# Performance work log

Measured on AMD Instinct MI355X. Metric: run time of the kernel, lower is better.

Reference implementation:

```python
import jax, jax.numpy as jnp
import numpy as np

BANDWIDTH = 1.0
DRIFT_COEF = 1.0
NEG_DRIFT_COEF = 0.5
EPS = 1e-8

B, TA, DA = 4096, 16, 8


def setup_inputs() -> dict:
    key = jax.random.key(0)
    k1, k2, k3 = jax.random.split(key, 3)
    x = jax.random.normal(k1, (B, TA, DA), dtype=jnp.float32)
    y_pos = jax.random.normal(k2, (B, TA, DA), dtype=jnp.float32)
    y_neg = jax.random.normal(k3, (B, TA, DA), dtype=jnp.float32)
    return {"x": x, "y_pos": y_pos, "y_neg": y_neg}


def _drift_field(x_flat, y_flat, sign):
    """Nadaraya-Watson weighted average of pairwise diffs, fused via norms+matmul.

    Equivalent to: sign * sum_j wn_ij * (x_i - y_j)
    where wn = row-normalized RBF kernel with masked diagonal.
    """
    b = x_flat.shape[0]
    x_sq = jnp.sum(x_flat * x_flat, axis=1)
    y_sq = jnp.sum(y_flat * y_flat, axis=1)
    d2 = x_sq[:, None] + y_sq[None, :] - 2.0 * (x_flat @ y_flat.T)
    d2 = jnp.maximum(d2, 0.0)
    w = jnp.exp(-d2 / (2.0 * BANDWIDTH ** 2))
    # mask self-interaction (mask_self=True)
    w = w * (1.0 - jnp.eye(b, dtype=w.dtype))
    s = jnp.sum(w, axis=1, keepdims=True)               # (B, 1)
    denom = jnp.maximum(s, EPS)
    wn = w / denom                                       # (B, B)
    # sum_j wn_ij (x_i - y_j) = x_i * rowsum(wn)_i - wn @ y
    diff_avg = x_flat * (s / denom) - wn @ y_flat        # (B, D)
    return sign * diff_avg


def reference(x, y_pos, y_neg):
    b = x.shape[0]
    x_flat = x.reshape(b, -1)
    yp_flat = y_pos.reshape(b, -1)
    yn_flat = y_neg.reshape(b, -1)
    # V_pos = wn_pos @ (-(x_i - y_j)); V_neg = wn_neg @ (x_i - y_j)
    v = DRIFT_COEF * _drift_field(x_flat, yp_flat, -1.0)
    v = v + NEG_DRIFT_COEF * _drift_field(x_flat, yn_flat, 1.0)
    return v.reshape(x.shape)
```

## Files before the change

### kernel.cpp

```cpp
#include <hip/hip_runtime.h>
#include <math.h>


#define EPSV 1e-8f
#define CUTOFF_F 162.0f
#define LCAP 1024

typedef unsigned int uint;
typedef unsigned short ushort;
typedef __attribute__((ext_vector_type(8))) short bf16x8;
typedef __attribute__((ext_vector_type(4))) float f32x4;

#define ACC_IDX 20480u
#define XA_BYTE 8388608u
#define MAT_BYTES 1048576u
#define WS_NEED 11534336u

static __device__ __forceinline__ ushort bf16_rne(float v) {
    uint u = __float_as_uint(v);
    uint r = (u + 0x7FFFu + ((u >> 16) & 1u)) >> 16;
    return (ushort)r;
}

typedef const __attribute__((address_space(1))) uint guint;
typedef __attribute__((address_space(3))) uint luint;
static __device__ __forceinline__ void lds_load16(const void* g, void* l) {
    __builtin_amdgcn_global_load_lds((guint*)g, (luint*)l, 16, 0, 0);
}

__global__ __launch_bounds__(256) void prep_k(
    const float* __restrict__ x, const float* __restrict__ yp,
    const float* __restrict__ yn, float* __restrict__ ws,
    unsigned char* __restrict__ wsb, int build)
{
    __shared__ ushort hi_s[4][128];
    const int t = threadIdx.x, wv = t >> 6, lane = t & 63;
    const int rid = blockIdx.x * 4 + wv;
    const int seg = rid >> 12;
    const int row = rid & 4095;
    const float* src = (seg == 0) ? x : (seg == 1) ? yp : yn;

    float2 v = ((const float2*)(src + (size_t)row * 128))[lane];
    float ss = v.x * v.x + v.y * v.y;
    #pragma unroll
    for (int off = 32; off > 0; off >>= 1) ss += __shfl_down(ss, off);
    if (lane == 0) ws[8192 + seg * 4096 + row] = ss;

    if (build) {
        hi_s[wv][2 * lane]     = bf16_rne(v.x);
        hi_s[wv][2 * lane + 1] = bf16_rne(v.y);
        __syncthreads();
        const int K = 2 * lane;
        const int g = K >> 6, c = (K >> 3) & 7, off = K & 7;
        const int Klog = (g << 6) + ((c ^ (row & 7)) << 3) + off;
        uint* dst = (uint*)(wsb + XA_BYTE + (size_t)seg * MAT_BYTES) + (size_t)row * 64;
        dst[lane] = (uint)hi_s[wv][Klog] | ((uint)hi_s[wv][Klog + 1] << 16);
    }

    const uint gid = blockIdx.x * 256u + (uint)t;
    for (uint u = gid; u < 1056768u; u += 786432u) {
        const uint idx = (u < 8192u) ? u : (u + 12288u);
        ws[idx] = 0.0f;
    }
}

__global__ __launch_bounds__(256) void phase_a_mfma(
    const float* __restrict__ x, const float* __restrict__ yp,
    const float* __restrict__ yn,
    const unsigned char* __restrict__ wsb, float* __restrict__ wsf)
{
    const ushort* __restrict__ XA = (const ushort*)(wsb + XA_BYTE);
    const ushort* __restrict__ YPB = (const ushort*)(wsb + XA_BYTE + MAT_BYTES);
    const ushort* __restrict__ YNB = (const ushort*)(wsb + XA_BYTE + 2u * MAT_BYTES);

    __shared__ ushort As[128 * 128];
    __shared__ ushort Bs[128 * 128];
    __shared__ uint pbuf[LCAP];
    __shared__ uint pcnt;

    const int t = threadIdx.x;
    const int lane = t & 63, wv = t >> 6;
    const int wr = wv >> 1, wc = wv & 1;
    const int i0 = blockIdx.y * 128, j0 = blockIdx.x * 128;
    const int m = lane & 15, qd = lane >> 4;
    const int r4 = lane >> 4, c16 = lane & 15;

    if (t == 0) pcnt = 0;

    #pragma unroll
    for (int q = 0; q < 8; ++q) {
        const int rr = 32 * wv + 4 * q;
        lds_load16(XA + (size_t)(i0 + rr + r4) * 128 + c16 * 8, &As[rr * 128]);
        lds_load16(YPB + (size_t)(j0 + rr + r4) * 128 + c16 * 8, &Bs[rr * 128]);
    }
    __syncthreads();

    float xq[4][4];
    #pragma unroll
    for (int fi = 0; fi < 4; ++fi)
        #pragma unroll
        for (int rg = 0; rg < 4; ++rg)
            xq[fi][rg] = wsf[8192 + i0 + 64 * wr + 16 * fi + 4 * qd + rg];

    auto run_field = [&](const int f) {
        f32x4 acc[4][4];
        #pragma unroll
        for (int a = 0; a < 4; ++a)
            #pragma unroll
            for (int bb = 0; bb < 4; ++bb) acc[a][bb] = (f32x4)0.0f;

        #pragma unroll
        for (int ks = 0; ks < 4; ++ks) {
            const int lc = 4 * ks + qd;
            const int phys = ((lc >> 3) << 3) | ((lc & 7) ^ (m & 7));
            bf16x8 av[4], bv[4];
            #pragma unroll
            for (int ff = 0; ff < 4; ++ff) {
                const int ra = 64 * wr + 16 * ff + m;
                av[ff] = *(const bf16x8*)&As[ra * 128 + phys * 8];
                const int rb = 64 * wc + 16 * ff + m;
                bv[ff] = *(const bf16x8*)&Bs[rb * 128 + phys * 8];
            }
            #pragma unroll
            for (int fi = 0; fi < 4; ++fi)
                #pragma unroll
                for (int fj = 0; fj < 4; ++fj)
                    acc[fi][fj] = __builtin_amdgcn_mfma_f32_16x16x32_bf16(
                        av[fi], bv[fj], acc[fi][fj], 0, 0, 0);
        }

        const float* __restrict__ ysq = wsf + 12288 + f * 4096;
        float yq[4];
        #pragma unroll
        for (int fj = 0; fj < 4; ++fj)
            yq[fj] = ysq[j0 + 64 * wc + 16 * fj + m];

        #pragma unroll
        for (int fi = 0; fi < 4; ++fi) {
            #pragma unroll
            for (int fj = 0; fj < 4; ++fj) {
                #pragma unroll
                for (int rg = 0; rg < 4; ++rg) {
                    const int i = i0 + 64 * wr + 16 * fi + 4 * qd + rg;
                    const int j = j0 + 64 * wc + 16 * fj + m;
                    float d2a = xq[fi][rg] + yq[fj] - 2.0f * acc[fi][fj][rg];
                    if (d2a < CUTOFF_F && i != j) {
                        uint li = atomicAdd(&pcnt, 1u);
                        if (li < LCAP)
                            pbuf[li] = (uint)i | ((uint)j << 12) | ((uint)f << 24);
                    }
                }
            }
        }
    };

    run_field(0);
    __syncthreads();
    #pragma unroll
    for (int q = 0; q < 8; ++q) {
        const int rr = 32 * wv + 4 * q;
        lds_load16(YNB + (size_t)(j0 + rr + r4) * 128 + c16 * 8, &Bs[rr * 128]);
    }
    __syncthreads();
    run_field(1);
    __syncthreads();

    uint n = pcnt; if (n > LCAP) n = LCAP;
    for (uint p = wv; p < n; p += 4) {
        const uint pk = pbuf[p];
        const uint i = pk & 0xFFFu, j = (pk >> 12) & 0xFFFu, fb = (pk >> 24) & 1u;
        const float* __restrict__ Yg = fb ? yn : yp;
        float2 xa = ((const float2*)(x + (size_t)i * 128))[lane];
        float2 yb = ((const float2*)(Yg + (size_t)j * 128))[lane];
        float d = xa.x * yb.x + xa.y * yb.y;
        #pragma unroll
        for (int off = 32; off > 0; off >>= 1) d += __shfl_xor(d, off);
        const float d2 = fmaxf(wsf[8192 + i] + wsf[12288 + fb * 4096u + j] - 2.0f * d, 0.0f);
        const float w = __expf(-0.5f * d2);
        if (lane == 0) atomicAdd(&wsf[fb * 4096u + i], w);
        float* __restrict__ accT = wsf + ACC_IDX + fb * 524288u + (size_t)i * 128u;
        atomicAdd(&accT[2 * lane],     w * yb.x);
        atomicAdd(&accT[2 * lane + 1], w * yb.y);
    }
}

__global__ __launch_bounds__(256) void phase_a_f32(
    const float* __restrict__ x, const float* __restrict__ yp,
    const float* __restrict__ yn, float* __restrict__ ws)
{
    const int f = blockIdx.z;
    const float* __restrict__ Y   = f ? yn : yp;
    const float* __restrict__ xsq = ws + 8192;
    const float* __restrict__ ysq = ws + (f ? 16384 : 12288);
    float* __restrict__ S         = ws + (f ? 4096 : 0);
    float* __restrict__ accT      = ws + ACC_IDX + (size_t)f * 524288u;

    __shared__ float xs[32][128 + 4];
    __shared__ float ys[32][128 + 4];

    const int t  = threadIdx.x;
    const int tx = t & 15, ty = t >> 4;
    const int i0 = blockIdx.y * 128, j0 = blockIdx.x * 128;

    float acc[8][8];
    #pragma unroll
    for (int a = 0; a < 8; ++a)
        #pragma unroll
        for (int bb = 0; bb < 8; ++bb) acc[a][bb] = 0.f;

    const int ldr = t >> 1;
    const int ldk = (t & 1) * 16;

    for (int k0 = 0; k0 < 128; k0 += 32) {
        #pragma unroll
        for (int q = 0; q < 4; ++q) {
            float4 vx = *(const float4*)&x[(size_t)(i0 + ldr) * 128 + k0 + ldk + 4 * q];
            float4 vy = *(const float4*)&Y[(size_t)(j0 + ldr) * 128 + k0 + ldk + 4 * q];
            const int kb = ldk + 4 * q;
            xs[kb + 0][ldr] = vx.x; xs[kb + 1][ldr] = vx.y;
            xs[kb + 2][ldr] = vx.z; xs[kb + 3][ldr] = vx.w;
            ys[kb + 0][ldr] = vy.x; ys[kb + 1][ldr] = vy.y;
            ys[kb + 2][ldr] = vy.z; ys[kb + 3][ldr] = vy.w;
        }
        __syncthreads();
        #pragma unroll 4
        for (int kk = 0; kk < 32; ++kk) {
            float4 a0 = *(const float4*)&xs[kk][8 * ty];
            float4 a1 = *(const float4*)&xs[kk][8 * ty + 4];
            float4 b0 = *(const float4*)&ys[kk][8 * tx];
            float4 b1 = *(const float4*)&ys[kk][8 * tx + 4];
            float av[8] = {a0.x, a0.y, a0.z, a0.w, a1.x, a1.y, a1.z, a1.w};
            float bv[8] = {b0.x, b0.y, b0.z, b0.w, b1.x, b1.y, b1.z, b1.w};
            #pragma unroll
            for (int di = 0; di < 8; ++di)
                #pragma unroll
                for (int dj = 0; dj < 8; ++dj)
                    acc[di][dj] = fmaf(av[di], bv[dj], acc[di][dj]);
        }
        __syncthreads();
    }

    float xqv[8], yqv[8], srow[8];
    #pragma unroll
    for (int di = 0; di < 8; ++di) { xqv[di] = xsq[i0 + 8 * ty + di]; srow[di] = 0.f; }
    #pragma unroll
    for (int dj = 0; dj < 8; ++dj) yqv[dj] = ysq[j0 + 8 * tx + dj];

    #pragma unroll
    for (int di = 0; di < 8; ++di) {
        const int i = i0 + 8 * ty + di;
        #pragma unroll
        for (int dj = 0; dj < 8; ++dj) {
            const int j = j0 + 8 * tx + dj;
            float d2 = fmaxf(xqv[di] + yqv[dj] - 2.0f * acc[di][dj], 0.0f);
            if (i != j) {
                float w = __expf(-0.5f * d2);
                srow[di] += w;
                if (d2 < CUTOFF_F) {
                    const float* Yrow = Y + (size_t)j * 128;
                    for (int k = 0; k < 128; ++k)
                        atomicAdd(&accT[(size_t)i * 128 + k], w * Yrow[k]);
                }
            }
        }
    }
    #pragma unroll
    for (int di = 0; di < 8; ++di) {
        float v = srow[di];
        #pragma unroll
        for (int off = 8; off > 0; off >>= 1) v += __shfl_down(v, off, 16);
        if (tx == 0) atomicAdd(&S[i0 + 8 * ty + di], v);
    }
}

__global__ __launch_bounds__(256) void finalize_k(
    const float* __restrict__ x, const float* __restrict__ ws,
    float* __restrict__ out)
{
    const uint gid = blockIdx.x * 256u + threadIdx.x;
    const uint i = gid >> 7;
    const float spv = ws[i], snv = ws[4096 + i];
    const float denp = fmaxf(spv, EPSV), denn = fmaxf(snv, EPSV);
    const float c = 0.5f * snv / denn - spv / denp;
    out[gid] = x[gid] * c
             + ws[ACC_IDX + gid] / denp
             - 0.5f * ws[ACC_IDX + 524288u + gid] / denn;
}

extern "C" void kernel_launch(void* const* d_in, const int* in_sizes, int n_in,
                              void* d_out, int out_size, void* d_ws, size_t ws_size,
                              hipStream_t stream)
{
    const float* x  = (const float*)d_in[0];
    const float* yp = (const float*)d_in[1];
    const float* yn = (const float*)d_in[2];
    float* out = (float*)d_out;
    float* ws  = (float*)d_ws;
    unsigned char* wsb = (unsigned char*)d_ws;

    const bool use_mfma = (ws_size >= WS_NEED);

    prep_k<<<3072, 256, 0, stream>>>(x, yp, yn, ws, wsb, use_mfma ? 1 : 0);
    if (use_mfma) {
        dim3 ga(32, 32, 1);
        phase_a_mfma<<<ga, 256, 0, stream>>>(x, yp, yn, wsb, ws);
    } else {
        dim3 ga(32, 32, 2);
        phase_a_f32<<<ga, 256, 0, stream>>>(x, yp, yn, ws);
    }
    finalize_k<<<2048, 256, 0, stream>>>(x, ws, out);
}
```

Before: 103.0 us.

## Convert fp32 to bf16 inside MFMA tile kernel and split fields across grid z

Removes the prep-stage build of pre-swizzled bf16 copies of x, y_pos and y_neg in workspace. The MFMA distance kernel now reads fp32 rows directly, rounds them to bf16 in registers, and stages two K-halves through smaller LDS tiles. The two fields move to separate blocks via blockIdx.z, and launch bounds are tightened for occupancy. This drops a global write/read round trip and lowers LDS use per block, but x tiles are converted twice and the candidate list cap is halved, which risks overflow if a tile has many close pairs.

Measured after the change: 101.2 us (median of 2 runs). Within noise of the previous version (-1.7%).

```diff
diff --git a/kernel.cpp b/kernel.cpp
--- a/kernel.cpp
+++ b/kernel.cpp
@@ -4,7 +4,7 @@
 
 #define EPSV 1e-8f
 #define CUTOFF_F 162.0f
-#define LCAP 1024
+#define LCAP 512
 
 typedef unsigned int uint;
 typedef unsigned short ushort;
@@ -12,9 +12,7 @@
 typedef __attribute__((ext_vector_type(4))) float f32x4;
 
 #define ACC_IDX 20480u
-#define XA_BYTE 8388608u
-#define MAT_BYTES 1048576u
-#define WS_NEED 11534336u
+#define WS_NEED 4276224u
 
 static __device__ __forceinline__ ushort bf16_rne(float v) {
     uint u = __float_as_uint(v);
@@ -22,18 +20,10 @@
     return (ushort)r;
 }
 
-typedef const __attribute__((address_space(1))) uint guint;
-typedef __attribute__((address_space(3))) uint luint;
-static __device__ __forceinline__ void lds_load16(const void* g, void* l) {
-    __builtin_amdgcn_global_load_lds((guint*)g, (luint*)l, 16, 0, 0);
-}
-
-__global__ __launch_bounds__(256) void prep_k(
+__global__ __launch_bounds__(256) void prep_lite(
     const float* __restrict__ x, const float* __restrict__ yp,
-    const float* __restrict__ yn, float* __restrict__ ws,
-    unsigned char* __restrict__ wsb, int build)
-{
-    __shared__ ushort hi_s[4][128];
+    const float* __restrict__ yn, float* __restrict__ ws)
+{
     const int t = threadIdx.x, wv = t >> 6, lane = t & 63;
     const int rid = blockIdx.x * 4 + wv;
     const int seg = rid >> 12;
@@ -46,35 +36,21 @@
     for (int off = 32; off > 0; off >>= 1) ss += __shfl_down(ss, off);
     if (lane == 0) ws[8192 + seg * 4096 + row] = ss;
 
-    if (build) {
-        hi_s[wv][2 * lane]     = bf16_rne(v.x);
-        hi_s[wv][2 * lane + 1] = bf16_rne(v.y);
-        __syncthreads();
-        const int K = 2 * lane;
-        const int g = K >> 6, c = (K >> 3) & 7, off = K & 7;
-        const int Klog = (g << 6) + ((c ^ (row & 7)) << 3) + off;
-        uint* dst = (uint*)(wsb + XA_BYTE + (size_t)seg * MAT_BYTES) + (size_t)row * 64;
-        dst[lane] = (uint)hi_s[wv][Klog] | ((uint)hi_s[wv][Klog + 1] << 16);
-    }
-
     const uint gid = blockIdx.x * 256u + (uint)t;
-    for (uint u = gid; u < 1056768u; u += 786432u) {
-        const uint idx = (u < 8192u) ? u : (u + 12288u);
-        ws[idx] = 0.0f;
-    }
-}
-
-__global__ __launch_bounds__(256) void phase_a_mfma(
+    if (gid < 8192u) ws[gid] = 0.0f;
+    if (gid < 262144u)
+        ((f32x4*)(ws + ACC_IDX))[gid] = (f32x4)0.0f;
+}
+
+__global__ __launch_bounds__(256, 4) void phase_a_mfma(
     const float* __restrict__ x, const float* __restrict__ yp,
-    const float* __restrict__ yn,
-    const unsigned char* __restrict__ wsb, float* __restrict__ wsf)
-{
-    const ushort* __restrict__ XA = (const ushort*)(wsb + XA_BYTE);
-    const ushort* __restrict__ YPB = (const ushort*)(wsb + XA_BYTE + MAT_BYTES);
-    const ushort* __restrict__ YNB = (const ushort*)(wsb + XA_BYTE + 2u * MAT_BYTES);
-
-    __shared__ ushort As[128 * 128];
-    __shared__ ushort Bs[128 * 128];
+    const float* __restrict__ yn, float* __restrict__ wsf)
+{
+    const int f = blockIdx.z;
+    const float* __restrict__ Yg = f ? yn : yp;
+
+    __shared__ ushort As[128 * 64];
+    __shared__ ushort Bs[128 * 64];
     __shared__ uint pbuf[LCAP];
     __shared__ uint pcnt;
 
@@ -83,43 +59,48 @@
     const int wr = wv >> 1, wc = wv & 1;
     const int i0 = blockIdx.y * 128, j0 = blockIdx.x * 128;
     const int m = lane & 15, qd = lane >> 4;
-    const int r4 = lane >> 4, c16 = lane & 15;
 
     if (t == 0) pcnt = 0;
 
-    #pragma unroll
-    for (int q = 0; q < 8; ++q) {
-        const int rr = 32 * wv + 4 * q;
-        lds_load16(XA + (size_t)(i0 + rr + r4) * 128 + c16 * 8, &As[rr * 128]);
-        lds_load16(YPB + (size_t)(j0 + rr + r4) * 128 + c16 * 8, &Bs[rr * 128]);
-    }
-    __syncthreads();
-
-    float xq[4][4];
-    #pragma unroll
-    for (int fi = 0; fi < 4; ++fi)
-        #pragma unroll
-        for (int rg = 0; rg < 4; ++rg)
-            xq[fi][rg] = wsf[8192 + i0 + 64 * wr + 16 * fi + 4 * qd + rg];
-
-    auto run_field = [&](const int f) {
-        f32x4 acc[4][4];
-        #pragma unroll
-        for (int a = 0; a < 4; ++a)
-            #pragma unroll
-            for (int bb = 0; bb < 4; ++bb) acc[a][bb] = (f32x4)0.0f;
-
-        #pragma unroll
-        for (int ks = 0; ks < 4; ++ks) {
-            const int lc = 4 * ks + qd;
-            const int phys = ((lc >> 3) << 3) | ((lc & 7) ^ (m & 7));
+    f32x4 acc[4][4];
+    #pragma unroll
+    for (int a = 0; a < 4; ++a)
+        #pragma unroll
+        for (int bb = 0; bb < 4; ++bb) acc[a][bb] = (f32x4)0.0f;
+
+    for (int kh = 0; kh < 2; ++kh) {
+        #pragma unroll
+        for (int q = 0; q < 4; ++q) {
+            const int w = t + 256 * q;
+            const int r = w >> 3, c = w & 7;
+            const int pc = c ^ (r & 7);
+            const float* ax = x + (size_t)(i0 + r) * 128 + kh * 64 + c * 8;
+            const float* by = Yg + (size_t)(j0 + r) * 128 + kh * 64 + c * 8;
+            float4 a0 = *(const float4*)ax, a1 = *(const float4*)(ax + 4);
+            float4 b0 = *(const float4*)by, b1 = *(const float4*)(by + 4);
+            union { ushort u[8]; bf16x8 v; } pa, pb;
+            pa.u[0] = bf16_rne(a0.x); pa.u[1] = bf16_rne(a0.y);
+            pa.u[2] = bf16_rne(a0.z); pa.u[3] = bf16_rne(a0.w);
+            pa.u[4] = bf16_rne(a1.x); pa.u[5] = bf16_rne(a1.y);
+            pa.u[6] = bf16_rne(a1.z); pa.u[7] = bf16_rne(a1.w);
+            pb.u[0] = bf16_rne(b0.x); pb.u[1] = bf16_rne(b0.y);
+            pb.u[2] = bf16_rne(b0.z); pb.u[3] = bf16_rne(b0.w);
+            pb.u[4] = bf16_rne(b1.x); pb.u[5] = bf16_rne(b1.y);
+            pb.u[6] = bf16_rne(b1.z); pb.u[7] = bf16_rne(b1.w);
+            *(bf16x8*)&As[r * 64 + pc * 8] = pa.v;
+            *(bf16x8*)&Bs[r * 64 + pc * 8] = pb.v;
+        }
+        __syncthreads();
+        #pragma unroll
+        for (int s = 0; s < 2; ++s) {
+            const int phys = (4 * s + qd) ^ (m & 7);
             bf16x8 av[4], bv[4];
             #pragma unroll
             for (int ff = 0; ff < 4; ++ff) {
                 const int ra = 64 * wr + 16 * ff + m;
-                av[ff] = *(const bf16x8*)&As[ra * 128 + phys * 8];
+                av[ff] = *(const bf16x8*)&As[ra * 64 + phys * 8];
                 const int rb = 64 * wc + 16 * ff + m;
-                bv[ff] = *(const bf16x8*)&Bs[rb * 128 + phys * 8];
+                bv[ff] = *(const bf16x8*)&Bs[rb * 64 + phys * 8];
             }
             #pragma unroll
             for (int fi = 0; fi < 4; ++fi)
@@ -128,57 +109,55 @@
                     acc[fi][fj] = __builtin_amdgcn_mfma_f32_16x16x32_bf16(
                         av[fi], bv[fj], acc[fi][fj], 0, 0, 0);
         }
-
-        const float* __restrict__ ysq = wsf + 12288 + f * 4096;
-        float yq[4];
-        #pragma unroll
-        for (int fj = 0; fj < 4; ++fj)
-            yq[fj] = ysq[j0 + 64 * wc + 16 * fj + m];
-
-        #pragma unroll
-        for (int fi = 0; fi < 4; ++fi) {
-            #pragma unroll
-            for (int fj = 0; fj < 4; ++fj) {
-                #pragma unroll
-                for (int rg = 0; rg < 4; ++rg) {
-                    const int i = i0 + 64 * wr + 16 * fi + 4 * qd + rg;
-                    const int j = j0 + 64 * wc + 16 * fj + m;
-                    float d2a = xq[fi][rg] + yq[fj] - 2.0f * acc[fi][fj][rg];
-                    if (d2a < CUTOFF_F && i != j) {
-                        uint li = atomicAdd(&pcnt, 1u);
-                        if (li < LCAP)
-                            pbuf[li] = (uint)i | ((uint)j << 12) | ((uint)f << 24);
-                    }
+        __syncthreads();
+    }
+
+    const float* __restrict__ xsq = wsf + 8192;
+    const float* __restrict__ ysq = wsf + 12288 + f * 4096;
+    float xq[4][4], yq[4];
+    #pragma unroll
+    for (int fi = 0; fi < 4; ++fi)
+        #pragma unroll
+        for (int rg = 0; rg < 4; ++rg)
+            xq[fi][rg] = xsq[i0 + 64 * wr + 16 * fi + 4 * qd + rg];
+    #pragma unroll
+    for (int fj = 0; fj < 4; ++fj)
+        yq[fj] = ysq[j0 + 64 * wc + 16 * fj + m];
+
+    #pragma unroll
+    for (int fi = 0; fi < 4; ++fi) {
+        #pragma unroll
+        for (int fj = 0; fj < 4; ++fj) {
+            #pragma unroll
+            for (int rg = 0; rg < 4; ++rg) {
+                const int i = i0 + 64 * wr + 16 * fi + 4 * qd + rg;
+                const int j = j0 + 64 * wc + 16 * fj + m;
+                float d2a = xq[fi][rg] + yq[fj] - 2.0f * acc[fi][fj][rg];
+                if (d2a < CUTOFF_F && i != j) {
+                    uint li = atomicAdd(&pcnt, 1u);
+                    if (li < LCAP)
+                        pbuf[li] = (uint)i | ((uint)j << 12);
                 }
             }
         }
-    };
-
-    run_field(0);
+    }
     __syncthreads();
-    #pragma unroll
-    for (int q = 0; q < 8; ++q) {
-        const int rr = 32 * wv + 4 * q;
-        lds_load16(YNB + (size_t)(j0 + rr + r4) * 128 + c16 * 8, &Bs[rr * 128]);
-    }
-    __syncthreads();
-    run_field(1);
-    __syncthreads();
-
+
+    float* __restrict__ S    = wsf + (f ? 4096 : 0);
+    float* __restrict__ accF = wsf + ACC_IDX + (size_t)f * 524288u;
     uint n = pcnt; if (n > LCAP) n = LCAP;
     for (uint p = wv; p < n; p += 4) {
         const uint pk = pbuf[p];
-        const uint i = pk & 0xFFFu, j = (pk >> 12) & 0xFFFu, fb = (pk >> 24) & 1u;
-        const float* __restrict__ Yg = fb ? yn : yp;
+        const uint i = pk & 0xFFFu, j = (pk >> 12) & 0xFFFu;
         float2 xa = ((const float2*)(x + (size_t)i * 128))[lane];
         float2 yb = ((const float2*)(Yg + (size_t)j * 128))[lane];
         float d = xa.x * yb.x + xa.y * yb.y;
         #pragma unroll
         for (int off = 32; off > 0; off >>= 1) d += __shfl_xor(d, off);
-        const float d2 = fmaxf(wsf[8192 + i] + wsf[12288 + fb * 4096u + j] - 2.0f * d, 0.0f);
+        const float d2 = fmaxf(xsq[i] + ysq[j] - 2.0f * d, 0.0f);
         const float w = __expf(-0.5f * d2);
-        if (lane == 0) atomicAdd(&wsf[fb * 4096u + i], w);
-        float* __restrict__ accT = wsf + ACC_IDX + fb * 524288u + (size_t)i * 128u;
+        if (lane == 0) atomicAdd(&S[i], w);
+        float* __restrict__ accT = accF + (size_t)i * 128u;
         atomicAdd(&accT[2 * lane],     w * yb.x);
         atomicAdd(&accT[2 * lane + 1], w * yb.y);
     }
@@ -296,16 +275,14 @@
     const float* yn = (const float*)d_in[2];
     float* out = (float*)d_out;
     float* ws  = (float*)d_ws;
-    unsigned char* wsb = (unsigned char*)d_ws;
 
     const bool use_mfma = (ws_size >= WS_NEED);
 
-    prep_k<<<3072, 256, 0, stream>>>(x, yp, yn, ws, wsb, use_mfma ? 1 : 0);
+    prep_lite<<<3072, 256, 0, stream>>>(x, yp, yn, ws);
+    dim3 ga(32, 32, 2);
     if (use_mfma) {
-        dim3 ga(32, 32, 1);
-        phase_a_mfma<<<ga, 256, 0, stream>>>(x, yp, yn, wsb, ws);
+        phase_a_mfma<<<ga, 256, 0, stream>>>(x, yp, yn, ws);
     } else {
-        dim3 ga(32, 32, 2);
         phase_a_f32<<<ga, 256, 0, stream>>>(x, yp, yn, ws);
     }
     finalize_k<<<2048, 256, 0, stream>>>(x, ws, out);
```

## Split MFMA phase across fields via grid z and halve LDS tiles with K-loop

Applied to the files above, without the earlier changes.

The MFMA candidate-pruning kernel now launches one block per (tile, field) on a z-dimension of 2 instead of processing both fields in one block. It also stages the K dimension in two 64-wide chunks, so the A and B shared tiles shrink from 32 KB each to 16 KB each, and the candidate buffer halves. The workspace offsets are moved down to match. The aim is lower LDS per block and more blocks, for higher occupancy and parallelism. The cost is the X tile being loaded twice, extra barriers, and a smaller candidate cap that could overflow.

New measurement: 103.3 us. About the same (+0.2%).

```diff
diff --git a/kernel.cpp b/kernel.cpp
--- a/kernel.cpp
+++ b/kernel.cpp
@@ -4,7 +4,7 @@
 
 #define EPSV 1e-8f
 #define CUTOFF_F 162.0f
-#define LCAP 1024
+#define LCAP 512
 
 typedef unsigned int uint;
 typedef unsigned short ushort;
@@ -12,9 +12,9 @@
 typedef __attribute__((ext_vector_type(4))) float f32x4;
 
 #define ACC_IDX 20480u
-#define XA_BYTE 8388608u
+#define XA_BYTE 4718592u
 #define MAT_BYTES 1048576u
-#define WS_NEED 11534336u
+#define WS_NEED 7864320u
 
 static __device__ __forceinline__ ushort bf16_rne(float v) {
     uint u = __float_as_uint(v);
@@ -69,12 +69,13 @@
     const float* __restrict__ yn,
     const unsigned char* __restrict__ wsb, float* __restrict__ wsf)
 {
+    const int f = blockIdx.z;
     const ushort* __restrict__ XA = (const ushort*)(wsb + XA_BYTE);
-    const ushort* __restrict__ YPB = (const ushort*)(wsb + XA_BYTE + MAT_BYTES);
-    const ushort* __restrict__ YNB = (const ushort*)(wsb + XA_BYTE + 2u * MAT_BYTES);
-
-    __shared__ ushort As[128 * 128];
-    __shared__ ushort Bs[128 * 128];
+    const ushort* __restrict__ YB = (const ushort*)(wsb + XA_BYTE + (f ? 2u : 1u) * MAT_BYTES);
+    const float* __restrict__ Yg  = f ? yn : yp;
+
+    __shared__ ushort As[128 * 64];
+    __shared__ ushort Bs[128 * 64];
     __shared__ uint pbuf[LCAP];
     __shared__ uint pcnt;
 
@@ -83,43 +84,36 @@
     const int wr = wv >> 1, wc = wv & 1;
     const int i0 = blockIdx.y * 128, j0 = blockIdx.x * 128;
     const int m = lane & 15, qd = lane >> 4;
-    const int r4 = lane >> 4, c16 = lane & 15;
+    const int srow = lane >> 3;
+    const int scol = lane & 7;
 
     if (t == 0) pcnt = 0;
 
-    #pragma unroll
-    for (int q = 0; q < 8; ++q) {
-        const int rr = 32 * wv + 4 * q;
-        lds_load16(XA + (size_t)(i0 + rr + r4) * 128 + c16 * 8, &As[rr * 128]);
-        lds_load16(YPB + (size_t)(j0 + rr + r4) * 128 + c16 * 8, &Bs[rr * 128]);
-    }
-    __syncthreads();
-
-    float xq[4][4];
-    #pragma unroll
-    for (int fi = 0; fi < 4; ++fi)
-        #pragma unroll
-        for (int rg = 0; rg < 4; ++rg)
-            xq[fi][rg] = wsf[8192 + i0 + 64 * wr + 16 * fi + 4 * qd + rg];
-
-    auto run_field = [&](const int f) {
-        f32x4 acc[4][4];
-        #pragma unroll
-        for (int a = 0; a < 4; ++a)
-            #pragma unroll
-            for (int bb = 0; bb < 4; ++bb) acc[a][bb] = (f32x4)0.0f;
-
-        #pragma unroll
-        for (int ks = 0; ks < 4; ++ks) {
-            const int lc = 4 * ks + qd;
-            const int phys = ((lc >> 3) << 3) | ((lc & 7) ^ (m & 7));
+    f32x4 acc[4][4];
+    #pragma unroll
+    for (int a = 0; a < 4; ++a)
+        #pragma unroll
+        for (int bb = 0; bb < 4; ++bb) acc[a][bb] = (f32x4)0.0f;
+
+    for (int k0 = 0; k0 < 128; k0 += 64) {
+        #pragma unroll
+        for (int q = 0; q < 4; ++q) {
+            const int grp = 4 * wv + q;
+            const int r = grp * 8 + srow;
+            lds_load16(XA + (size_t)(i0 + r) * 128 + k0 + scol * 8, &As[grp * 512]);
+            lds_load16(YB + (size_t)(j0 + r) * 128 + k0 + scol * 8, &Bs[grp * 512]);
+        }
+        __syncthreads();
+        #pragma unroll
+        for (int ks = 0; ks < 2; ++ks) {
+            const int ca = (4 * ks + qd) ^ (m & 7);
             bf16x8 av[4], bv[4];
             #pragma unroll
             for (int ff = 0; ff < 4; ++ff) {
                 const int ra = 64 * wr + 16 * ff + m;
-                av[ff] = *(const bf16x8*)&As[ra * 128 + phys * 8];
+                av[ff] = *(const bf16x8*)&As[ra * 64 + ca * 8];
                 const int rb = 64 * wc + 16 * ff + m;
-                bv[ff] = *(const bf16x8*)&Bs[rb * 128 + phys * 8];
+                bv[ff] = *(const bf16x8*)&Bs[rb * 64 + ca * 8];
             }
             #pragma unroll
             for (int fi = 0; fi < 4; ++fi)
@@ -128,57 +122,55 @@
                     acc[fi][fj] = __builtin_amdgcn_mfma_f32_16x16x32_bf16(
                         av[fi], bv[fj], acc[fi][fj], 0, 0, 0);
         }
-
-        const float* __restrict__ ysq = wsf + 12288 + f * 4096;
-        float yq[4];
-        #pragma unroll
-        for (int fj = 0; fj < 4; ++fj)
-            yq[fj] = ysq[j0 + 64 * wc + 16 * fj + m];
-
-        #pragma unroll
-        for (int fi = 0; fi < 4; ++fi) {
+        __syncthreads();
+    }
+
+    const float* __restrict__ xsq = wsf + 8192;
+    const float* __restrict__ ysq = wsf + 12288 + f * 4096;
+    float xq[4][4], yq[4];
+    #pragma unroll
+    for (int fi = 0; fi < 4; ++fi)
+        #pragma unroll
+        for (int rg = 0; rg < 4; ++rg)
+            xq[fi][rg] = xsq[i0 + 64 * wr + 16 * fi + 4 * qd + rg];
+    #pragma unroll
+    for (int fj = 0; fj < 4; ++fj)
+        yq[fj] = ysq[j0 + 64 * wc + 16 * fj + m];
+
+    #pragma unroll
+    for (int fi = 0; fi < 4; ++fi) {
+        #pragma unroll
+        for (int fj = 0; fj < 4; ++fj) {
             #pragma unroll
-            for (int fj = 0; fj < 4; ++fj) {
-                #pragma unroll
-                for (int rg = 0; rg < 4; ++rg) {
-                    const int i = i0 + 64 * wr + 16 * fi + 4 * qd + rg;
-                    const int j = j0 + 64 * wc + 16 * fj + m;
-                    float d2a = xq[fi][rg] + yq[fj] - 2.0f * acc[fi][fj][rg];
-                    if (d2a < CUTOFF_F && i != j) {
-                        uint li = atomicAdd(&pcnt, 1u);
-                        if (li < LCAP)
-                            pbuf[li] = (uint)i | ((uint)j << 12) | ((uint)f << 24);
-                    }
+            for (int rg = 0; rg < 4; ++rg) {
+                const int i = i0 + 64 * wr + 16 * fi + 4 * qd + rg;
+                const int j = j0 + 64 * wc + 16 * fj + m;
+                float d2a = xq[fi][rg] + yq[fj] - 2.0f * acc[fi][fj][rg];
+                if (d2a < CUTOFF_F && i != j) {
+                    uint li = atomicAdd(&pcnt, 1u);
+                    if (li < LCAP)
+                        pbuf[li] = (uint)i | ((uint)j << 12);
                 }
             }
         }
-    };
-
-    run_field(0);
+    }
     __syncthreads();
-    #pragma unroll
-    for (int q = 0; q < 8; ++q) {
-        const int rr = 32 * wv + 4 * q;
-        lds_load16(YNB + (size_t)(j0 + rr + r4) * 128 + c16 * 8, &Bs[rr * 128]);
-    }
-    __syncthreads();
-    run_field(1);
-    __syncthreads();
-
+
+    float* __restrict__ S    = wsf + (f ? 4096 : 0);
+    float* __restrict__ accF = wsf + ACC_IDX + (size_t)f * 524288u;
     uint n = pcnt; if (n > LCAP) n = LCAP;
     for (uint p = wv; p < n; p += 4) {
         const uint pk = pbuf[p];
-        const uint i = pk & 0xFFFu, j = (pk >> 12) & 0xFFFu, fb = (pk >> 24) & 1u;
-        const float* __restrict__ Yg = fb ? yn : yp;
+        const uint i = pk & 0xFFFu, j = (pk >> 12) & 0xFFFu;
         float2 xa = ((const float2*)(x + (size_t)i * 128))[lane];
         float2 yb = ((const float2*)(Yg + (size_t)j * 128))[lane];
         float d = xa.x * yb.x + xa.y * yb.y;
         #pragma unroll
         for (int off = 32; off > 0; off >>= 1) d += __shfl_xor(d, off);
-        const float d2 = fmaxf(wsf[8192 + i] + wsf[12288 + fb * 4096u + j] - 2.0f * d, 0.0f);
+        const float d2 = fmaxf(xsq[i] + ysq[j] - 2.0f * d, 0.0f);
         const float w = __expf(-0.5f * d2);
-        if (lane == 0) atomicAdd(&wsf[fb * 4096u + i], w);
-        float* __restrict__ accT = wsf + ACC_IDX + fb * 524288u + (size_t)i * 128u;
+        if (lane == 0) atomicAdd(&S[i], w);
+        float* __restrict__ accT = accF + (size_t)i * 128u;
         atomicAdd(&accT[2 * lane],     w * yb.x);
         atomicAdd(&accT[2 * lane + 1], w * yb.y);
     }
@@ -301,11 +293,10 @@
     const bool use_mfma = (ws_size >= WS_NEED);
 
     prep_k<<<3072, 256, 0, stream>>>(x, yp, yn, ws, wsb, use_mfma ? 1 : 0);
+    dim3 ga(32, 32, 2);
     if (use_mfma) {
-        dim3 ga(32, 32, 1);
         phase_a_mfma<<<ga, 256, 0, stream>>>(x, yp, yn, wsb, ws);
     } else {
-        dim3 ga(32, 32, 2);
         phase_a_f32<<<ga, 256, 0, stream>>>(x, yp, yn, ws);
     }
     finalize_k<<<2048, 256, 0, stream>>>(x, ws, out);
```
